# Performance work log

Measured on AMD Instinct MI355X. Metric: run time of the kernel, lower is better.

The kernel has to match this reference:

```python
import jax, jax.numpy as jnp
from jax import lax
import numpy as np

_MAX_SQRT_GRADIENT = 1000.0

@jax.custom_vjp
def sqrt_bound_derivative(x):
    return jnp.sqrt(x)

def _sbd_fwd(x):
    return jnp.sqrt(x), x

def _sbd_bwd(x, g):
    clipped = jnp.clip(4.0 * x, 1.0 / _MAX_SQRT_GRADIENT**2)
    return (g / jnp.sqrt(clipped),)

sqrt_bound_derivative.defvjp(_sbd_fwd, _sbd_bwd)

HIDDEN = 2560
LRU = 2560
HEADS = 10
CONV_W = 4
BATCH = 2
SEQ = 4096


def setup_inputs() -> dict:
    key = jax.random.key(0)
    ks = jax.random.split(key, 12)
    s = 0.02  # init scale for weights
    inp = {
        'input_states': jax.random.normal(ks[0], (BATCH, SEQ, HIDDEN), jnp.float32),
        'position_ids': jnp.broadcast_to(jnp.arange(SEQ, dtype=jnp.int64), (BATCH, SEQ)),
        'prev_h': jnp.zeros((BATCH, LRU), jnp.float32),
        'w_y': jax.random.normal(ks[1], (LRU, HIDDEN), jnp.float32) * s,
        'b_y': jax.random.normal(ks[2], (LRU,), jnp.float32) * s,
        'w_x': jax.random.normal(ks[3], (LRU, HIDDEN), jnp.float32) * s,
        'b_x': jax.random.normal(ks[4], (LRU,), jnp.float32) * s,
        'w_out': jax.random.normal(ks[5], (HIDDEN, LRU), jnp.float32) * s,
        'b_out': jax.random.normal(ks[6], (HIDDEN,), jnp.float32) * s,
        'conv_w': jax.random.normal(ks[7], (LRU, CONV_W), jnp.float32) * 0.3,
        'conv_b': jax.random.normal(ks[8], (LRU,), jnp.float32) * s,
        'a_param': jax.random.normal(ks[9], (LRU,), jnp.float32),
        'ig_w': jax.random.normal(ks[10], (LRU // HEADS, LRU), jnp.float32) * s,
        'ig_b': jnp.zeros((LRU // HEADS,), jnp.float32),
        'ag_w': jax.random.normal(ks[11], (LRU // HEADS, LRU), jnp.float32) * s,
        'ag_b': jnp.zeros((LRU // HEADS,), jnp.float32),
    }
    return inp


def _block_gate(x_bshi, gate_w, gate_b, heads, bw):
    # gate_w is the nn.Linear weight [bw, heads*bw] reshaped to block-diagonal form
    w = gate_w.reshape(heads, bw, bw).transpose(0, 2, 1)  # h i j
    y = jnp.einsum('bshi,hij->bshj', x_bshi, w) + gate_b
    B, S = y.shape[0], y.shape[1]
    return jax.nn.sigmoid(y.reshape(B, S, heads * bw))


def _rglru(activations, position_ids, prev_h, a_param, ig_w, ig_b, ag_w, ag_b):
    B, S, D = activations.shape
    bw = ig_w.shape[0]
    heads = ig_w.shape[1] // bw
    reset = (position_ids[:, :, None] == 0)  # [B,S,1] bool
    x = activations.reshape(B, S, heads, bw)
    gate_x = _block_gate(x, ig_w, ig_b, heads, bw)  # [B,S,D]
    gate_a = _block_gate(x, ag_w, ag_b, heads, bw)  # [B,S,D]
    log_a = -8.0 * gate_a * jax.nn.softplus(a_param)
    a = jnp.exp(log_a)
    a_square = jnp.exp(2.0 * log_a)
    gated_x = activations * gate_x
    multiplier = sqrt_bound_derivative(1.0 - a_square)
    multiplier = jnp.where(reset, 1.0, multiplier)
    normalized_x = gated_x * multiplier.astype(activations.dtype)
    a = a * (~reset)  # zero the decay at document boundaries

    def step(h, inp):
        a_t, x_t = inp  # [B,D] each
        h = a_t.astype(jnp.float32) * h + x_t.astype(jnp.float32)
        return h, h.astype(activations.dtype)

    xs = (a.transpose(1, 0, 2), normalized_x.transpose(1, 0, 2))  # time-major
    last_h, y = lax.scan(step, prev_h, xs)
    return y.transpose(1, 0, 2), last_h


def reference(input_states, position_ids, prev_h, w_y, b_y, w_x, b_x,
              w_out, b_out, conv_w, conv_b, a_param, ig_w, ig_b, ag_w, ag_b):
    B, S, _ = input_states.shape
    # y branch: gelu(tanh approx)
    y_branch = jax.nn.gelu(input_states @ w_y.T + b_y, approximate=True)
    # x branch: linear + depthwise causal conv (kernel width CONV_W)
    x_branch = input_states @ w_x.T + b_x  # [B,S,LRU]
    Wd = conv_w.shape[1]
    xp = jnp.pad(x_branch, ((0, 0), (Wd - 1, 0), (0, 0)))
    conv_out = conv_b + sum(xp[:, k:k + S, :] * conv_w[:, k] for k in range(Wd))
    # RG-LRU
    h, last_h = _rglru(conv_out, position_ids, prev_h, a_param, ig_w, ig_b, ag_w, ag_b)
    h = h * y_branch
    out = h @ w_out.T + b_out
    return out
```

## Files before the change

kernel.cpp:

```cpp
#include <hip/hip_runtime.h>
#include <hip/hip_bf16.h>
#include <math.h>

typedef __hip_bfloat16 bf16;
typedef __attribute__((ext_vector_type(4))) float f32x4;
typedef __attribute__((ext_vector_type(8))) __bf16 bf16x8;

static constexpr int HID    = 2560;
static constexpr int LRUD   = 2560;
static constexpr int HEADSN = 10;
static constexpr int BWID   = 256;
static constexpr int SEQL   = 4096;
static constexpr int BATCHN = 2;
static constexpr int NTOK   = BATCHN * SEQL;
static constexpr int NCHUNK = 128;
static constexpr int CHLEN  = 32;

#define GAS __attribute__((address_space(1)))
#define LAS __attribute__((address_space(3)))
#define MEMFENCE asm volatile("" ::: "memory")
#define PHASE_SYNC                                        \
  __builtin_amdgcn_s_barrier(); MEMFENCE;                 \
  asm volatile("s_waitcnt lgkmcnt(0)" ::: "memory");
#define PHASE_END                                         \
  __builtin_amdgcn_s_barrier(); MEMFENCE;
#define VMGATE6 asm volatile("s_waitcnt vmcnt(6)" ::: "memory")
#define VMGATE0 asm volatile("s_waitcnt vmcnt(0)" ::: "memory")

__device__ __forceinline__ void async_copy16(void* lds, const void* g) {
  __builtin_amdgcn_global_load_lds((const GAS unsigned int*)g,
                                   (LAS unsigned int*)lds, 16, 0, 0);
}

template<int EPI>
__global__ __launch_bounds__(256, 2)
void gemm128q_kernel(const bf16* __restrict__ A, int lda,
                     const bf16* __restrict__ B0p, const bf16* __restrict__ B1p,
                     int ldb,
                     const float* __restrict__ bias0, const float* __restrict__ bias1,
                     void* __restrict__ out0, void* __restrict__ out1,
                     int ldc, int K)
{
  __shared__ __align__(16) bf16 As[2][128 * 64];
  __shared__ __align__(16) bf16 Bs[2][128 * 64];

  const int tid  = threadIdx.x;
  const int wave = tid >> 6;
  const int lane = tid & 63;
  const int wm   = wave >> 1;
  const int wn   = wave & 1;

  const int nxy  = gridDim.x * gridDim.y;
  const int orig = blockIdx.y * gridDim.x + blockIdx.x;
  const int swz  = (orig & 7) * (nxy >> 3) + (orig >> 3);
  const int m0   = (swz / gridDim.x) * 128;
  const int n0   = (swz % gridDim.x) * 128;

  const int zsel = (EPI == 1) ? (int)blockIdx.z : 0;
  const bf16*  Bw   = zsel ? B1p : B0p;
  const float* bias = zsel ? bias1 : bias0;

  const int NT = K / 64;
  f32x4  acc[4][4] = {};
  bf16x8 a[2][2], bl[2][2], bh[2][2];

  const int srow = tid >> 3;
  const int spb  = (tid & 7) * 16;
  const int scb  = spb ^ ((srow & 7) << 4);

  const int lrow = lane & 15;
  const int swzc = (lane & 7) << 4;
  const int col0 = ((lane >> 4) * 16) ^ swzc;
  const int col1 = (64 + (lane >> 4) * 16) ^ swzc;
  const char* aBase = (const char*)&As[0][0] + (wm * 64 + lrow) * 128;
  const char* bBase = (const char*)&Bs[0][0] + (wn * 64 + lrow) * 128;
  constexpr int BUFB = 128 * 64 * 2;

  auto stageA = [&](int t, int c) {
    const int r = c * 32 + srow;
    async_copy16(&As[t & 1][c * 2048 + wave * 512],
                 A + (size_t)(m0 + r) * lda + t * 64 + (scb >> 1));
  };
  auto stageB = [&](int t, int c) {
    const int r = c * 32 + srow;
    async_copy16(&Bs[t & 1][c * 2048 + wave * 512],
                 Bw + (size_t)(n0 + r) * ldb + t * 64 + (scb >> 1));
  };
  auto stA_lo = [&](int t) { stageA(t, 0); stageA(t, 2); };
  auto stA_hi = [&](int t) { stageA(t, 1); stageA(t, 3); };
  auto stB_lo = [&](int t) { stageB(t, 0); stageB(t, 2); };
  auto stB_hi = [&](int t) { stageB(t, 1); stageB(t, 3); };

  auto readAhalf = [&](int buf, int half) {
    const char* p = aBase + buf * BUFB + half * 2 * 2048;
#pragma unroll
    for (int j = 0; j < 2; ++j) {
      a[j][0] = *(const bf16x8*)(p + j * 2048 + col0);
      a[j][1] = *(const bf16x8*)(p + j * 2048 + col1);
    }
  };
  auto readBlo = [&](int buf) {
    const char* p = bBase + buf * BUFB;
#pragma unroll
    for (int f = 0; f < 2; ++f) {
      bl[f][0] = *(const bf16x8*)(p + f * 2048 + col0);
      bl[f][1] = *(const bf16x8*)(p + f * 2048 + col1);
    }
  };
  auto readBhi = [&](int buf) {
    const char* p = bBase + buf * BUFB + 2 * 2048;
#pragma unroll
    for (int f = 0; f < 2; ++f) {
      bh[f][0] = *(const bf16x8*)(p + f * 2048 + col0);
      bh[f][1] = *(const bf16x8*)(p + f * 2048 + col1);
    }
  };
  auto mfmaQ = [&](int fmB, int fnB, bf16x8 (&bx)[2][2]) {
#pragma unroll
    for (int ks = 0; ks < 2; ++ks)
#pragma unroll
      for (int fn = 0; fn < 2; ++fn)
#pragma unroll
        for (int fm = 0; fm < 2; ++fm)
          acc[fmB + fm][fnB + fn] = __builtin_amdgcn_mfma_f32_16x16x32_bf16(
              a[fm][ks], bx[fn][ks], acc[fmB + fm][fnB + fn], 0, 0, 0);
  };

  stA_lo(0); stB_lo(0); stB_hi(0); stA_hi(0);
  stA_lo(1); stB_lo(1); stB_hi(1);
  VMGATE6;
  PHASE_END;

  const int NI = NT / 2;
  for (int i = 0; i < NI; ++i) {
    const int  t0 = 2 * i, t1 = 2 * i + 1;
    const bool s2 = (t0 + 2) < NT;

    readAhalf(0, 0); readBlo(0);
    stA_hi(t1);
    PHASE_SYNC;
    __builtin_amdgcn_s_setprio(1); mfmaQ(0, 0, bl); __builtin_amdgcn_s_setprio(0);
    PHASE_END;
    readBhi(0);
    if (s2) stA_lo(t0 + 2);
    PHASE_SYNC;
    __builtin_amdgcn_s_setprio(1); mfmaQ(0, 2, bh); __builtin_amdgcn_s_setprio(0);
    PHASE_END;
    readAhalf(0, 1);
    if (s2) stB_lo(t0 + 2);
    PHASE_SYNC;
    __builtin_amdgcn_s_setprio(1); mfmaQ(2, 2, bh); __builtin_amdgcn_s_setprio(0);
    PHASE_END;
    if (s2) stB_hi(t0 + 2);
    PHASE_SYNC;
    __builtin_amdgcn_s_setprio(1); mfmaQ(2, 0, bl); __builtin_amdgcn_s_setprio(0);
    if (s2) { VMGATE6; } else { VMGATE0; }
    PHASE_END;
    readAhalf(1, 0); readBlo(1);
    if (s2) stA_hi(t0 + 2);
    PHASE_SYNC;
    __builtin_amdgcn_s_setprio(1); mfmaQ(0, 0, bl); __builtin_amdgcn_s_setprio(0);
    PHASE_END;
    readBhi(1);
    if (s2) stA_lo(t1 + 2);
    PHASE_SYNC;
    __builtin_amdgcn_s_setprio(1); mfmaQ(0, 2, bh); __builtin_amdgcn_s_setprio(0);
    PHASE_END;
    readAhalf(1, 1);
    if (s2) stB_lo(t1 + 2);
    PHASE_SYNC;
    __builtin_amdgcn_s_setprio(1); mfmaQ(2, 2, bh); __builtin_amdgcn_s_setprio(0);
    PHASE_END;
    if (s2) stB_hi(t1 + 2);
    PHASE_SYNC;
    __builtin_amdgcn_s_setprio(1); mfmaQ(2, 0, bl); __builtin_amdgcn_s_setprio(0);
    if (s2) { VMGATE6; }
    PHASE_END;
  }

  const int mrb = (lane >> 4) * 4;
  const int ncc = lane & 15;
#pragma unroll
  for (int fm = 0; fm < 4; ++fm) {
#pragma unroll
    for (int fn = 0; fn < 4; ++fn) {
      const int n  = n0 + wn * 64 + fn * 16 + ncc;
      const float bv = bias[n];
#pragma unroll
      for (int r = 0; r < 4; ++r) {
        const int m = m0 + wm * 64 + fm * 16 + mrb + r;
        const size_t idx = (size_t)m * ldc + n;
        float v = acc[fm][fn][r] + bv;
        if constexpr (EPI == 0) {
          ((float*)out0)[idx] = v;
        } else {
          if (zsel == 0) {
            const float t = tanhf(0.7978845608028654f * (v + 0.044715f * v * v * v));
            ((bf16*)out0)[idx] = __float2bfloat16(0.5f * v * (1.0f + t));
          } else {
            ((bf16*)out1)[idx] = __float2bfloat16(v);
          }
        }
      }
    }
  }
}

__global__ __launch_bounds__(256)
void gate_gemm_kernel(const bf16* __restrict__ Conv,
                      const bf16* __restrict__ IGb, const bf16* __restrict__ AGb,
                      const float* __restrict__ ig_b, const float* __restrict__ ag_b,
                      bf16* __restrict__ Gx, bf16* __restrict__ Ga)
{
  __shared__ __align__(16) bf16 As[128 * 64];
  __shared__ __align__(16) bf16 Bs[128 * 64];

  const int tid  = threadIdx.x;
  const int wave = tid >> 6;
  const int lane = tid & 63;
  const int wy   = wave >> 1;
  const int wx   = wave & 1;
  const int m0   = blockIdx.y * 128;
  const int n0   = blockIdx.x * 128;
  const int head = blockIdx.z % HEADSN;
  const int sel  = blockIdx.z / HEADSN;

  const bf16*  A    = Conv + head * BWID;
  const bf16*  Bw   = (sel ? AGb : IGb) + (size_t)head * BWID * BWID;
  const float* bias = sel ? ag_b : ig_b;
  bf16*        Cp   = (sel ? Ga : Gx) + head * BWID;

  f32x4 acc[4][4] = {};
  const int srow = tid >> 3;
  const int spb  = (tid & 7) * 16;
  const int scb  = spb ^ ((srow & 7) << 4);

  const int lrow = lane & 15;
  const int swzc = (lane & 7) << 4;
  const int col0 = ((lane >> 4) * 16) ^ swzc;
  const int col1 = (64 + (lane >> 4) * 16) ^ swzc;
  const char* aBase = (const char*)As + (wy * 64 + lrow) * 128;
  const char* bBase = (const char*)Bs + (wx * 64 + lrow) * 128;

  for (int k0 = 0; k0 < BWID; k0 += 64) {
#pragma unroll
    for (int rd = 0; rd < 4; ++rd) {
      const int r = rd * 32 + srow;
      async_copy16(&As[rd * 2048 + wave * 512],
                   A + (size_t)(m0 + r) * LRUD + k0 + (scb >> 1));
      async_copy16(&Bs[rd * 2048 + wave * 512],
                   Bw + (size_t)(n0 + r) * BWID + k0 + (scb >> 1));
    }
    __syncthreads();
#pragma unroll
    for (int ks = 0; ks < 2; ++ks) {
      const int colk = ks ? col1 : col0;
      bf16x8 af[4], bfr[4];
#pragma unroll
      for (int f = 0; f < 4; ++f) {
        af[f]  = *(const bf16x8*)(aBase + f * 2048 + colk);
        bfr[f] = *(const bf16x8*)(bBase + f * 2048 + colk);
      }
#pragma unroll
      for (int fm = 0; fm < 4; ++fm)
#pragma unroll
        for (int fn = 0; fn < 4; ++fn)
          acc[fm][fn] = __builtin_amdgcn_mfma_f32_16x16x32_bf16(af[fm], bfr[fn], acc[fm][fn], 0, 0, 0);
    }
    __syncthreads();
  }

  const int mrb = (lane >> 4) * 4;
  const int ncc = lane & 15;
#pragma unroll
  for (int fm = 0; fm < 4; ++fm) {
#pragma unroll
    for (int fn = 0; fn < 4; ++fn) {
      const int n  = n0 + wx * 64 + fn * 16 + ncc;
      const float bv = bias[n];
#pragma unroll
      for (int r = 0; r < 4; ++r) {
        const int m = m0 + wy * 64 + fm * 16 + mrb + r;
        float v = acc[fm][fn][r] + bv;
        Cp[(size_t)m * LRUD + n] = __float2bfloat16(1.0f / (1.0f + expf(-v)));
      }
    }
  }
}

static constexpr int CV0 = NTOK * HID / 4;
static constexpr int CVW = LRUD * HID / 4;
static constexpr int CVG = BWID * LRUD / 4;
static constexpr int CVT_TOTAL = CV0 + 3 * CVW + 2 * CVG;

__device__ __forceinline__ void cvt4(const float* src, bf16* dst, int j) {
  const float4 v = *(const float4*)(src + (size_t)j * 4);
  dst[(size_t)j * 4 + 0] = __float2bfloat16(v.x);
  dst[(size_t)j * 4 + 1] = __float2bfloat16(v.y);
  dst[(size_t)j * 4 + 2] = __float2bfloat16(v.z);
  dst[(size_t)j * 4 + 3] = __float2bfloat16(v.w);
}

__global__ __launch_bounds__(256)
void cvt_all_kernel(const float* __restrict__ x_in, const float* __restrict__ w_y,
                    const float* __restrict__ w_x, const float* __restrict__ w_out,
                    const float* __restrict__ ig_w, const float* __restrict__ ag_w,
                    bf16* __restrict__ Xbf, bf16* __restrict__ Wyb,
                    bf16* __restrict__ Wxb, bf16* __restrict__ Wob,
                    bf16* __restrict__ IGb, bf16* __restrict__ AGb)
{
  int g = blockIdx.x * 256 + threadIdx.x;
  if (g < CV0)                       { cvt4(x_in,  Xbf, g); return; }
  g -= CV0;
  if (g < CVW)                       { cvt4(w_y,   Wyb, g); return; }
  g -= CVW;
  if (g < CVW)                       { cvt4(w_x,   Wxb, g); return; }
  g -= CVW;
  if (g < CVW)                       { cvt4(w_out, Wob, g); return; }
  g -= CVW;
  if (g < CVG)                       { cvt4(ig_w,  IGb, g); return; }
  g -= CVG;
  cvt4(ag_w, AGb, g);
}

__global__ __launch_bounds__(256)
void conv_kernel(const bf16* __restrict__ Xb, const float* __restrict__ cw,
                 const float* __restrict__ cbias, bf16* __restrict__ out) {
  const int c  = blockIdx.x * 256 + threadIdx.x;
  const int t0 = blockIdx.y * 8;
  const int bb = blockIdx.z;
  size_t base = ((size_t)bb * SEQL + t0) * LRUD + c;
  const float w0 = cw[c * 4 + 0], w1 = cw[c * 4 + 1];
  const float w2 = cw[c * 4 + 2], w3 = cw[c * 4 + 3];
  const float bc = cbias[c];
  float xm1, xm2, xm3;
  if (blockIdx.y == 0) { xm1 = xm2 = xm3 = 0.f; }
  else {
    xm1 = __bfloat162float(Xb[base - (size_t)LRUD]);
    xm2 = __bfloat162float(Xb[base - (size_t)2 * LRUD]);
    xm3 = __bfloat162float(Xb[base - (size_t)3 * LRUD]);
  }
#pragma unroll
  for (int tl = 0; tl < 8; ++tl) {
    const float x = __bfloat162float(Xb[base]);
    out[base] = __float2bfloat16(bc + x * w3 + xm1 * w2 + xm2 * w1 + xm3 * w0);
    xm3 = xm2; xm2 = xm1; xm1 = x;
    base += LRUD;
  }
}

__device__ __forceinline__ void compute_ax(float conv, float gx, float ga, float sp,
                                           int t, float& a, float& x) {
  const float la  = -8.f * ga * sp;
  a               = expf(la);
  const float asq = expf(2.f * la);
  float mult      = sqrtf(fmaxf(1.f - asq, 0.f));
  if (t == 0) { a = 0.f; mult = 1.f; }
  x = conv * gx * mult;
}

__global__ __launch_bounds__(256)
void scan1_kernel(const bf16* __restrict__ conv, const bf16* __restrict__ gxb,
                  const bf16* __restrict__ gab, const float* __restrict__ a_param,
                  float* __restrict__ cA, float* __restrict__ cX) {
  const int c     = blockIdx.x * 256 + threadIdx.x;
  const int chunk = blockIdx.y;
  const int b     = blockIdx.z;
  const float ap  = a_param[c];
  const float sp  = (ap > 20.f) ? ap : log1pf(expf(ap));
  size_t base = ((size_t)b * SEQL + (size_t)chunk * CHLEN) * LRUD + c;
  float A = 1.f, X = 0.f;
  for (int tl = 0; tl < CHLEN; ++tl) {
    float a, x;
    compute_ax(__bfloat162float(conv[base]), __bfloat162float(gxb[base]),
               __bfloat162float(gab[base]), sp, chunk * CHLEN + tl, a, x);
    X = a * X + x;
    A *= a;
    base += LRUD;
  }
  const size_t ci = ((size_t)b * NCHUNK + chunk) * LRUD + c;
  cA[ci] = A;
  cX[ci] = X;
}

__global__ __launch_bounds__(256)
void scan2_kernel(const float* __restrict__ cA, const float* __restrict__ cX,
                  const float* __restrict__ prev_h, float* __restrict__ pref) {
  const int g = blockIdx.x * 256 + threadIdx.x;
  const int b = g / LRUD;
  const int c = g % LRUD;
  float h = prev_h[g];
#pragma unroll 8
  for (int ch = 0; ch < NCHUNK; ++ch) {
    const size_t ci = ((size_t)b * NCHUNK + ch) * LRUD + c;
    pref[ci] = h;
    h = cA[ci] * h + cX[ci];
  }
}

__global__ __launch_bounds__(256)
void scan3_kernel(const bf16* __restrict__ conv, const bf16* __restrict__ gxb,
                  const bf16* __restrict__ gab, const float* __restrict__ a_param,
                  const float* __restrict__ pref, const bf16* __restrict__ yb,
                  bf16* __restrict__ hm) {
  const int c     = blockIdx.x * 256 + threadIdx.x;
  const int chunk = blockIdx.y;
  const int b     = blockIdx.z;
  const float ap  = a_param[c];
  const float sp  = (ap > 20.f) ? ap : log1pf(expf(ap));
  float h = pref[((size_t)b * NCHUNK + chunk) * LRUD + c];
  size_t base = ((size_t)b * SEQL + (size_t)chunk * CHLEN) * LRUD + c;
  for (int tl = 0; tl < CHLEN; ++tl) {
    float a, x;
    compute_ax(__bfloat162float(conv[base]), __bfloat162float(gxb[base]),
               __bfloat162float(gab[base]), sp, chunk * CHLEN + tl, a, x);
    h = a * h + x;
    hm[base] = __float2bfloat16(h * __bfloat162float(yb[base]));
    base += LRUD;
  }
}

extern "C" void kernel_launch(void* const* d_in, const int* in_sizes, int n_in,
                              void* d_out, int out_size, void* d_ws, size_t ws_size,
                              hipStream_t stream) {
  const float* x_in    = (const float*)d_in[0];
  const float* prev_h  = (const float*)d_in[2];
  const float* w_y     = (const float*)d_in[3];
  const float* b_y     = (const float*)d_in[4];
  const float* w_x     = (const float*)d_in[5];
  const float* b_x     = (const float*)d_in[6];
  const float* w_out   = (const float*)d_in[7];
  const float* b_out   = (const float*)d_in[8];
  const float* conv_w  = (const float*)d_in[9];
  const float* conv_b  = (const float*)d_in[10];
  const float* a_param = (const float*)d_in[11];
  const float* ig_w    = (const float*)d_in[12];
  const float* ig_b    = (const float*)d_in[13];
  const float* ag_w    = (const float*)d_in[14];
  const float* ag_b    = (const float*)d_in[15];

  char* ws = (char*)d_ws;
  size_t off = 0;
  auto alloc = [&](size_t bytes) -> char* {
    char* p = ws + off;
    off += (bytes + 255) & ~(size_t)255;
    return p;
  };
  bf16*  Xbf  = (bf16*)alloc((size_t)NTOK * HID * 2);
  bf16*  Wyb  = (bf16*)alloc((size_t)LRUD * HID * 2);
  bf16*  Wxb  = (bf16*)alloc((size_t)LRUD * HID * 2);
  bf16*  Wob  = (bf16*)alloc((size_t)HID * LRUD * 2);
  bf16*  IGb  = (bf16*)alloc((size_t)BWID * LRUD * 2);
  bf16*  AGb  = (bf16*)alloc((size_t)BWID * LRUD * 2);
  bf16*  Conv = (bf16*)alloc((size_t)NTOK * LRUD * 2);
  float* cA   = (float*)alloc((size_t)BATCHN * NCHUNK * LRUD * 4);
  float* cX   = (float*)alloc((size_t)BATCHN * NCHUNK * LRUD * 4);
  float* pref = (float*)alloc((size_t)BATCHN * NCHUNK * LRUD * 4);

  bf16* Yb = (bf16*)d_out;
  bf16* Xb = (bf16*)d_out + (size_t)NTOK * LRUD;
  bf16* Gx = Xbf;
  bf16* Ga = Xb;
  bf16* Hm = Conv;

  cvt_all_kernel<<<dim3(CVT_TOTAL / 256), 256, 0, stream>>>(
      x_in, w_y, w_x, w_out, ig_w, ag_w, Xbf, Wyb, Wxb, Wob, IGb, AGb);

  gemm128q_kernel<1><<<dim3(LRUD / 128, NTOK / 128, 2), 256, 0, stream>>>(
      Xbf, HID, Wyb, Wxb, HID, b_y, b_x, Yb, Xb, LRUD, HID);
  conv_kernel<<<dim3(LRUD / 256, SEQL / 8, BATCHN), 256, 0, stream>>>(
      Xb, conv_w, conv_b, Conv);
  gate_gemm_kernel<<<dim3(BWID / 128, NTOK / 128, 2 * HEADSN), 256, 0, stream>>>(
      Conv, IGb, AGb, ig_b, ag_b, Gx, Ga);
  scan1_kernel<<<dim3(LRUD / 256, NCHUNK, BATCHN), 256, 0, stream>>>(
      Conv, Gx, Ga, a_param, cA, cX);
  scan2_kernel<<<dim3((BATCHN * LRUD) / 256), 256, 0, stream>>>(cA, cX, prev_h, pref);
  scan3_kernel<<<dim3(LRUD / 256, NCHUNK, BATCHN), 256, 0, stream>>>(
      Conv, Gx, Ga, a_param, pref, Yb, Hm);
  gemm128q_kernel<0><<<dim3(HID / 128, NTOK / 128), 256, 0, stream>>>(
      Hm, LRUD, Wob, Wob, LRUD, b_out, b_out, (float*)d_out, (float*)d_out,
      HID, LRUD);

  (void)in_sizes; (void)n_in; (void)out_size; (void)ws_size;
}
```

Baseline: 555.9 us.

## Use 256x256-tile 8-wave GEMM with phased LDS pipeline for input projections

Adds a new GEMM kernel with 256x256 output tiles, 512 threads and a double-buffered LDS pipeline. The pipeline interleaves async global-to-LDS staging with quarter-tile MFMA phases under barriers and s_setprio. It replaces the 128x128 kernel for the fused y/x input projection GEMM, cutting global traffic per flop and raising data reuse. In exchange it uses much more LDS (128KB per block) and many more registers, and the larger tiles give fewer blocks, which may hurt occupancy and wave-count balance.

```diff
diff --git a/kernel.cpp b/kernel.cpp
--- a/kernel.cpp
+++ b/kernel.cpp
@@ -26,10 +26,187 @@
   __builtin_amdgcn_s_barrier(); MEMFENCE;
 #define VMGATE6 asm volatile("s_waitcnt vmcnt(6)" ::: "memory")
 #define VMGATE0 asm volatile("s_waitcnt vmcnt(0)" ::: "memory")
+#define LGKM8   asm volatile("s_waitcnt lgkmcnt(8)" ::: "memory")
 
 __device__ __forceinline__ void async_copy16(void* lds, const void* g) {
   __builtin_amdgcn_global_load_lds((const GAS unsigned int*)g,
                                    (LAS unsigned int*)lds, 16, 0, 0);
+}
+
+template<int EPI>
+__global__ __launch_bounds__(512, 2)
+void gemm256_kernel(const bf16* __restrict__ A, int lda,
+                    const bf16* __restrict__ B0p, const bf16* __restrict__ B1p,
+                    int ldb,
+                    const float* __restrict__ bias0, const float* __restrict__ bias1,
+                    void* __restrict__ out0, void* __restrict__ out1,
+                    int ldc, int K)
+{
+  __shared__ __align__(16) bf16 As[2][256 * 64];
+  __shared__ __align__(16) bf16 Bs[2][256 * 64];
+
+  const int tid  = threadIdx.x;
+  const int wave = tid >> 6;
+  const int lane = tid & 63;
+  const int wm   = wave >> 2;
+  const int wn   = wave & 3;
+
+  const int nxy  = gridDim.x * gridDim.y;
+  const int orig = blockIdx.y * gridDim.x + blockIdx.x;
+  const int swz  = (orig & 7) * (nxy >> 3) + (orig >> 3);
+  const int m0   = (swz / gridDim.x) * 256;
+  const int n0   = (swz % gridDim.x) * 256;
+
+  const int zsel = (EPI == 1) ? (int)blockIdx.z : 0;
+  const bf16*  Bw   = zsel ? B1p : B0p;
+  const float* bias = zsel ? bias1 : bias0;
+
+  const int NT = K / 64;
+  f32x4  acc[8][4] = {};
+  bf16x8 a[4][2], bl[2][2], bh[2][2];
+
+  const int srow = tid >> 3;
+  const int spb  = (tid & 7) * 16;
+  const int scb  = spb ^ ((srow & 7) << 4);
+
+  const int lrow = lane & 15;
+  const int swzc = (lane & 7) << 4;
+  const int col0 = ((lane >> 4) * 16) ^ swzc;
+  const int col1 = (64 + (lane >> 4) * 16) ^ swzc;
+  const char* aBase = (const char*)&As[0][0] + (wm * 128 + lrow) * 128;
+  const char* bBase = (const char*)&Bs[0][0] + (wn * 64 + lrow) * 128;
+  constexpr int BUFB = 256 * 64 * 2;
+
+  auto stageA = [&](int t, int c) {
+    const int r = c * 64 + srow;
+    async_copy16(&As[t & 1][c * 4096 + wave * 512],
+                 A + (size_t)(m0 + r) * lda + t * 64 + (scb >> 1));
+  };
+  auto stageB = [&](int t, int c) {
+    const int r = c * 64 + srow;
+    async_copy16(&Bs[t & 1][c * 4096 + wave * 512],
+                 Bw + (size_t)(n0 + r) * ldb + t * 64 + (scb >> 1));
+  };
+  auto stA_lo = [&](int t) { stageA(t, 0); stageA(t, 2); };
+  auto stA_hi = [&](int t) { stageA(t, 1); stageA(t, 3); };
+  auto stB01  = [&](int t) { stageB(t, 0); stageB(t, 1); };
+  auto stB23  = [&](int t) { stageB(t, 2); stageB(t, 3); };
+
+  auto readAhalf = [&](int buf, int half) {
+    const char* p = aBase + buf * BUFB + half * 4 * 2048;
+#pragma unroll
+    for (int j = 0; j < 4; ++j) {
+      a[j][0] = *(const bf16x8*)(p + j * 2048 + col0);
+      a[j][1] = *(const bf16x8*)(p + j * 2048 + col1);
+    }
+  };
+  auto readBlo = [&](int buf) {
+    const char* p = bBase + buf * BUFB;
+#pragma unroll
+    for (int f = 0; f < 2; ++f) {
+      bl[f][0] = *(const bf16x8*)(p + f * 2048 + col0);
+      bl[f][1] = *(const bf16x8*)(p + f * 2048 + col1);
+    }
+  };
+  auto readBhi = [&](int buf) {
+    const char* p = bBase + buf * BUFB + 2 * 2048;
+#pragma unroll
+    for (int f = 0; f < 2; ++f) {
+      bh[f][0] = *(const bf16x8*)(p + f * 2048 + col0);
+      bh[f][1] = *(const bf16x8*)(p + f * 2048 + col1);
+    }
+  };
+  auto mfmaQ = [&](int fmB, int fnB, bf16x8 (&bx)[2][2]) {
+#pragma unroll
+    for (int ks = 0; ks < 2; ++ks)
+#pragma unroll
+      for (int fn = 0; fn < 2; ++fn)
+#pragma unroll
+        for (int fm = 0; fm < 4; ++fm)
+          acc[fmB + fm][fnB + fn] = __builtin_amdgcn_mfma_f32_16x16x32_bf16(
+              a[fm][ks], bx[fn][ks], acc[fmB + fm][fnB + fn], 0, 0, 0);
+  };
+
+  stA_lo(0); stB01(0); stB23(0); stA_hi(0);
+  stA_lo(1); stB01(1); stB23(1);
+  VMGATE6;
+  PHASE_END;
+
+  const int NI = NT / 2;
+  for (int i = 0; i < NI; ++i) {
+    const int  t0 = 2 * i, t1 = 2 * i + 1;
+    const bool s2 = (t0 + 2) < NT;
+
+    readAhalf(0, 0); readBlo(0);
+    stA_hi(t1);
+    LGKM8;
+    PHASE_SYNC;
+    __builtin_amdgcn_s_setprio(1); mfmaQ(0, 0, bl); __builtin_amdgcn_s_setprio(0);
+    PHASE_END;
+    readBhi(0);
+    if (s2) stA_lo(t0 + 2);
+    PHASE_SYNC;
+    __builtin_amdgcn_s_setprio(1); mfmaQ(0, 2, bh); __builtin_amdgcn_s_setprio(0);
+    PHASE_END;
+    readAhalf(0, 1);
+    if (s2) stB01(t0 + 2);
+    PHASE_SYNC;
+    __builtin_amdgcn_s_setprio(1); mfmaQ(4, 2, bh); __builtin_amdgcn_s_setprio(0);
+    PHASE_END;
+    if (s2) stB23(t0 + 2);
+    PHASE_SYNC;
+    __builtin_amdgcn_s_setprio(1); mfmaQ(4, 0, bl); __builtin_amdgcn_s_setprio(0);
+    if (s2) { VMGATE6; } else { VMGATE0; }
+    PHASE_END;
+    readAhalf(1, 0); readBlo(1);
+    if (s2) stA_hi(t0 + 2);
+    LGKM8;
+    PHASE_SYNC;
+    __builtin_amdgcn_s_setprio(1); mfmaQ(0, 0, bl); __builtin_amdgcn_s_setprio(0);
+    PHASE_END;
+    readBhi(1);
+    if (s2) stA_lo(t1 + 2);
+    PHASE_SYNC;
+    __builtin_amdgcn_s_setprio(1); mfmaQ(0, 2, bh); __builtin_amdgcn_s_setprio(0);
+    PHASE_END;
+    readAhalf(1, 1);
+    if (s2) stB01(t1 + 2);
+    PHASE_SYNC;
+    __builtin_amdgcn_s_setprio(1); mfmaQ(4, 2, bh); __builtin_amdgcn_s_setprio(0);
+    PHASE_END;
+    if (s2) stB23(t1 + 2);
+    PHASE_SYNC;
+    __builtin_amdgcn_s_setprio(1); mfmaQ(4, 0, bl); __builtin_amdgcn_s_setprio(0);
+    if (s2) { VMGATE6; }
+    PHASE_END;
+  }
+
+  const int mrb = (lane >> 4) * 4;
+  const int ncc = lane & 15;
+#pragma unroll
+  for (int fm = 0; fm < 8; ++fm) {
+#pragma unroll
+    for (int fn = 0; fn < 4; ++fn) {
+      const int n  = n0 + wn * 64 + fn * 16 + ncc;
+      const float bv = bias[n];
+#pragma unroll
+      for (int r = 0; r < 4; ++r) {
+        const int m = m0 + wm * 128 + fm * 16 + mrb + r;
+        const size_t idx = (size_t)m * ldc + n;
+        float v = acc[fm][fn][r] + bv;
+        if constexpr (EPI == 0) {
+          ((float*)out0)[idx] = v;
+        } else {
+          if (zsel == 0) {
+            const float t = tanhf(0.7978845608028654f * (v + 0.044715f * v * v * v));
+            ((bf16*)out0)[idx] = __float2bfloat16(0.5f * v * (1.0f + t));
+          } else {
+            ((bf16*)out1)[idx] = __float2bfloat16(v);
+          }
+        }
+      }
+    }
+  }
 }
 
 template<int EPI>
@@ -466,7 +643,7 @@
   cvt_all_kernel<<<dim3(CVT_TOTAL / 256), 256, 0, stream>>>(
       x_in, w_y, w_x, w_out, ig_w, ag_w, Xbf, Wyb, Wxb, Wob, IGb, AGb);
 
-  gemm128q_kernel<1><<<dim3(LRUD / 128, NTOK / 128, 2), 256, 0, stream>>>(
+  gemm256_kernel<1><<<dim3(LRUD / 256, NTOK / 256, 2), 512, 0, stream>>>(
       Xbf, HID, Wyb, Wxb, HID, b_y, b_x, Yb, Xb, LRUD, HID);
   conv_kernel<<<dim3(LRUD / 256, SEQL / 8, BATCHN), 256, 0, stream>>>(
       Xb, conv_w, conv_b, Conv);
```

Measured after the change: 557.4 us. Within noise of the previous version (+0.3%).
